# Kernel tuning notes

Hardware: AMD Instinct MI355X
Metric: run time of the kernel (lower is better)

The kernel has to match this reference:

```python
import jax, jax.numpy as jnp
import numpy as np

SEQ, D_IN, D_OUT = 8192, 768, 64


def setup_inputs() -> dict:
    key = jax.random.key(0)
    kx, kq, kk, kv = jax.random.split(key, 4)
    scale = 1.0 / np.sqrt(D_IN)
    return {
        "x": jax.random.normal(kx, (SEQ, D_IN), dtype=jnp.float32),
        # torch Linear weight layout: [d_out, d_in]
        "W_Q": jax.random.uniform(kq, (D_OUT, D_IN), dtype=jnp.float32, minval=-scale, maxval=scale),
        "W_K": jax.random.uniform(kk, (D_OUT, D_IN), dtype=jnp.float32, minval=-scale, maxval=scale),
        "W_V": jax.random.uniform(kv, (D_OUT, D_IN), dtype=jnp.float32, minval=-scale, maxval=scale),
    }


def reference(x, W_Q, W_K, W_V):
    # q,k,v: [seq, d_out]
    q = x @ W_Q.T
    k = x @ W_K.T
    v = x @ W_V.T
    scores = (q @ k.T) / jnp.sqrt(jnp.asarray(k.shape[-1], x.dtype))  # [seq, seq]
    attn = jax.nn.softmax(scores, axis=-1)
    return attn @ v  # [seq, d_out]
```

## Files before the change

### kernel.cpp

```cpp
#include <hip/hip_runtime.h>
#include <hip/hip_bf16.h>
#include <math.h>

#define SEQ 8192
#define DIN 768
#define DOUT 64
#define QSCALE 0.1803368801111214f

typedef __attribute__((ext_vector_type(8))) short short8;
typedef __attribute__((ext_vector_type(4))) short short4v;
typedef __attribute__((ext_vector_type(4))) float floatx4;
typedef __attribute__((ext_vector_type(2))) unsigned int uint2v;

__device__ __forceinline__ void gload16(const void* g, void* l) {
    __builtin_amdgcn_global_load_lds(
        (const __attribute__((address_space(1))) unsigned int*)g,
        (__attribute__((address_space(3))) unsigned int*)l, 16, 0, 0);
}

__device__ __forceinline__ unsigned pack2(float a, float b) {
    __hip_bfloat162 h = __float22bfloat162_rn(make_float2(a, b));
    return *(unsigned*)&h;
}

__device__ __forceinline__ unsigned short bfbits(float f) {
    __hip_bfloat16 h = __float2bfloat16(f);
    return *(unsigned short*)&h;
}

__device__ __forceinline__ float exp2r(float x) {
#if __has_builtin(__builtin_amdgcn_exp2f)
    return __builtin_amdgcn_exp2f(x);
#else
    float r; asm("v_exp_f32 %0, %1" : "=v"(r) : "v"(x)); return r;
#endif
}

__device__ __forceinline__ floatx4 max4(floatx4 a, floatx4 b) {
    floatx4 r;
    r[0] = fmaxf(a[0], b[0]); r[1] = fmaxf(a[1], b[1]);
    r[2] = fmaxf(a[2], b[2]); r[3] = fmaxf(a[3], b[3]);
    return r;
}

__device__ __forceinline__ floatx4 mfma16(short4v a, short4v b, floatx4 c) {
#if __has_builtin(__builtin_amdgcn_mfma_f32_16x16x16bf16_1k)
    return __builtin_amdgcn_mfma_f32_16x16x16bf16_1k(a, b, c, 0, 0, 0);
#else
    asm("v_mfma_f32_16x16x16_bf16 %0, %1, %2, %0" : "+v"(c) : "v"(a), "v"(b));
    return c;
#endif
}

__global__ __launch_bounds__(256) void prep_w(
    const float* __restrict__ Wq, const float* __restrict__ Wk,
    const float* __restrict__ Wv, unsigned short* __restrict__ wbf)
{
    const int i = blockIdx.x * 256 + threadIdx.x;
    const int base = i * 8;
    const int row = base / DIN;
    const int k = base % DIN;
    const float* src = (row < 64)  ? &Wq[(size_t)row * DIN + k]
                     : (row < 128) ? &Wk[(size_t)(row - 64) * DIN + k]
                                   : &Wv[(size_t)(row - 128) * DIN + k];
    const float4 f0 = *(const float4*)src;
    const float4 f1 = *(const float4*)(src + 4);
    uint4 v;
    v.x = pack2(f0.x, f0.y);
    v.y = pack2(f0.z, f0.w);
    v.z = pack2(f1.x, f1.y);
    v.w = pack2(f1.z, f1.w);
    *(uint4*)&wbf[base] = v;
}

__global__ __launch_bounds__(512) void qkv_mfma(
    const float* __restrict__ x, const unsigned short* __restrict__ wbf,
    unsigned short* __restrict__ qbf, unsigned short* __restrict__ kbf,
    unsigned short* __restrict__ vtbf)
{
    __shared__ __align__(16) unsigned char xs[2][64 * 128];
    __shared__ __align__(16) unsigned char wsm[2][192 * 128];

    const int t = threadIdx.x;
    const int l = t & 63;
    const int wid = t >> 6;
    const int h = wid & 3;
    const int ntb = (wid >> 2) * 6;
    const int g = l >> 4;
    const int q4 = l & 15;
    const int row0 = blockIdx.x * 64;

    const int Rx_st = t >> 3;
    const int slx   = t & 7;
    const int Rr    = l >> 3;
    const int sld   = (l & 7) ^ Rr;

    floatx4 acc[6];
#pragma unroll
    for (int i = 0; i < 6; ++i) acc[i] = (floatx4){0.f, 0.f, 0.f, 0.f};

#define STAGE_X(buf, k0)                                                      \
    {                                                                         \
        const float4 a = *(const float4*)&x[(size_t)(row0 + Rx_st) * DIN + (k0) + slx * 8]; \
        const float4 b = *(const float4*)&x[(size_t)(row0 + Rx_st) * DIN + (k0) + slx * 8 + 4]; \
        uint4 v;                                                              \
        v.x = pack2(a.x, a.y); v.y = pack2(a.z, a.w);                         \
        v.z = pack2(b.x, b.y); v.w = pack2(b.z, b.w);                         \
        *(uint4*)&xs[buf][Rx_st * 128 + ((slx ^ (Rx_st & 7)) << 4)] = v;      \
    }

#define STAGE_W(buf, k0)                                                      \
    {                                                                         \
        _Pragma("unroll")                                                     \
        for (int ss = 0; ss < 3; ++ss) {                                      \
            const int s = wid * 3 + ss;                            \
            const int Rw = 8 * s + Rr;                            \
            gload16(&wbf[(size_t)Rw * DIN + (k0) + sld * 8], &wsm[buf][s * 1024]); \
        }                                                                     \
    }

    STAGE_X(0, 0)
    STAGE_W(0, 0)

    int cur = 0;
    for (int kc = 0; kc < 12; ++kc) {
        __syncthreads();

        float4 xa, xb;
        const bool more = (kc + 1 < 12);
        if (more) {
            const int k1 = (kc + 1) * 64;
            STAGE_W(cur ^ 1, k1)
            xa = *(const float4*)&x[(size_t)(row0 + Rx_st) * DIN + k1 + slx * 8];
            xb = *(const float4*)&x[(size_t)(row0 + Rx_st) * DIN + k1 + slx * 8 + 4];
        }

        __builtin_amdgcn_s_setprio(1);
#pragma unroll
        for (int ks = 0; ks < 2; ++ks) {
            const int sl = g + 4 * ks;
            const int Rx = h * 16 + q4;
            const short8 a = *(const short8*)&xs[cur][Rx * 128 + ((sl ^ (Rx & 7)) << 4)];
#pragma unroll
            for (int j = 0; j < 6; ++j) {
                const int Rw = (ntb + j) * 16 + q4;
                const short8 b = *(const short8*)&wsm[cur][Rw * 128 + ((sl ^ (Rw & 7)) << 4)];
                acc[j] = __builtin_amdgcn_mfma_f32_16x16x32_bf16(a, b, acc[j], 0, 0, 0);
            }
        }
        __builtin_amdgcn_s_setprio(0);

        if (more) {
            uint4 v;
            v.x = pack2(xa.x, xa.y); v.y = pack2(xa.z, xa.w);
            v.z = pack2(xb.x, xb.y); v.w = pack2(xb.z, xb.w);
            *(uint4*)&xs[cur ^ 1][Rx_st * 128 + ((slx ^ (Rx_st & 7)) << 4)] = v;
        }
        cur ^= 1;
    }

    const int rb = row0 + h * 16 + (g << 2);
#pragma unroll
    for (int j = 0; j < 6; ++j) {
        const int nt = ntb + j;
#pragma unroll
        for (int r = 0; r < 4; ++r) {
            const float v = acc[j][r];
            const int R = rb + r;
            if (nt < 4) {
                qbf[(size_t)R * 64 + nt * 16 + q4] = bfbits(v * QSCALE);
            } else if (nt < 8) {
                kbf[(size_t)R * 64 + (nt - 4) * 16 + q4] = bfbits(v);
            } else {
                vtbf[(size_t)((nt - 8) * 16 + q4) * SEQ + R] = bfbits(v);
            }
        }
    }
#undef STAGE_X
#undef STAGE_W
}

__global__ __launch_bounds__(256, 4) void flash_mfma(
    const unsigned short* __restrict__ qbf,
    const unsigned short* __restrict__ kbf,
    const unsigned short* __restrict__ vtbf,
    float* __restrict__ opart,
    float* __restrict__ ml,
    int nsplit, int direct)
{
    __shared__ __align__(16) unsigned char lds[32768];
    unsigned char* lkb = lds;
    unsigned char* lvb = lds + 16384;

    const int t = threadIdx.x;
    const int l = t & 63;
    const int g = l >> 4;
    const int q4 = l & 15;
    const int wid = t >> 6;
    const int row0 = blockIdx.x * 64;
    const int split = blockIdx.y;
    const int chunk = SEQ / nsplit;
    const int kbeg = split * chunk;
    const int NT = chunk / 64;

    short8 qf[2];
#pragma unroll
    for (int ks = 0; ks < 2; ++ks)
        qf[ks] = *(const short8*)&qbf[(size_t)(row0 + wid * 16 + q4) * 64 + (g + 4 * ks) * 8];

    {
        const int Rr = l >> 3;
        const int sl = (l & 7) ^ Rr;
#pragma unroll
        for (int ss = 0; ss < 2; ++ss) {
            const int s = wid * 2 + ss;
            const int R = 8 * s + Rr;
            gload16(&kbf[(size_t)(kbeg + R) * 64 + sl * 8], lkb + s * 1024);
            gload16(&vtbf[(size_t)R * SEQ + kbeg + sl * 8], lvb + s * 1024);
        }
    }
    __syncthreads();

    floatx4 oacc[4];
#pragma unroll
    for (int i = 0; i < 4; ++i) oacc[i] = (floatx4){0.f, 0.f, 0.f, 0.f};
    floatx4 l_acc = (floatx4){0.f, 0.f, 0.f, 0.f};
    float m_run = -INFINITY;

    int cur = 0;
    for (int tt = 0; tt < NT; ++tt) {
        const unsigned char* lk = lkb + cur * 8192;
        const unsigned char* lv = lvb + cur * 8192;

        if (tt + 1 < NT) {
            const int kt1 = kbeg + (tt + 1) * 64;
            const int Rr = l >> 3;
            const int sl = (l & 7) ^ Rr;
#pragma unroll
            for (int ss = 0; ss < 2; ++ss) {
                const int s = wid * 2 + ss;
                const int R = 8 * s + Rr;
                gload16(&kbf[(size_t)(kt1 + R) * 64 + sl * 8],
                        lkb + (cur ^ 1) * 8192 + s * 1024);
                gload16(&vtbf[(size_t)R * SEQ + kt1 + sl * 8],
                        lvb + (cur ^ 1) * 8192 + s * 1024);
            }
        }

        floatx4 sacc[4];
#pragma unroll
        for (int i = 0; i < 4; ++i) sacc[i] = (floatx4){0.f, 0.f, 0.f, 0.f};
        __builtin_amdgcn_s_setprio(1);
#pragma unroll
        for (int ks = 0; ks < 2; ++ks) {
            const int sl = g + 4 * ks;
#pragma unroll
            for (int nt = 0; nt < 4; ++nt) {
                const int R = nt * 16 + q4;
                const short8 kf = *(const short8*)&lk[R * 128 + ((sl ^ (R & 7)) << 4)];
                sacc[nt] = __builtin_amdgcn_mfma_f32_16x16x32_bf16(kf, qf[ks], sacc[nt], 0, 0, 0);
            }
        }
        __builtin_amdgcn_s_setprio(0);

        const floatx4 mm = max4(max4(sacc[0], sacc[1]), max4(sacc[2], sacc[3]));
        const float own = fmaxf(fmaxf(mm[0], mm[1]), fmaxf(mm[2], mm[3]));

        if (__any(own > m_run + 8.0f)) {
            float pm = own;
            pm = fmaxf(pm, __shfl_xor(pm, 16));
            pm = fmaxf(pm, __shfl_xor(pm, 32));
            const float mn = fmaxf(m_run, pm);
            const float alpha = exp2r(m_run - mn);
            m_run = mn;
            l_acc *= alpha;
#pragma unroll
            for (int dt = 0; dt < 4; ++dt) oacc[dt] *= alpha;
        }

        floatx4 pv4[4];
#pragma unroll
        for (int nt = 0; nt < 4; ++nt) {
            floatx4 d = sacc[nt];
            d[0] -= m_run; d[1] -= m_run; d[2] -= m_run; d[3] -= m_run;
            pv4[nt][0] = exp2r(d[0]); pv4[nt][1] = exp2r(d[1]);
            pv4[nt][2] = exp2r(d[2]); pv4[nt][3] = exp2r(d[3]);
        }
        l_acc += (pv4[0] + pv4[1]) + (pv4[2] + pv4[3]);

        __builtin_amdgcn_s_setprio(1);
#pragma unroll
        for (int kb = 0; kb < 4; ++kb) {
            const unsigned p0 = pack2(pv4[kb][0], pv4[kb][1]);
            const unsigned p1 = pack2(pv4[kb][2], pv4[kb][3]);
            const short4v bfr = __builtin_bit_cast(short4v, (uint2v){p0, p1});
            const int sl = kb * 2 + (g >> 1);
#pragma unroll
            for (int dt = 0; dt < 4; ++dt) {
                const int R = dt * 16 + q4;
                const short4v a = *(const short4v*)&lv[R * 128 +
                    ((sl ^ (R & 7)) << 4) + ((g & 1) << 3)];
                oacc[dt] = mfma16(a, bfr, oacc[dt]);
            }
        }
        __builtin_amdgcn_s_setprio(0);

        __syncthreads();
        cur ^= 1;
    }

    float l_run = (l_acc[0] + l_acc[1]) + (l_acc[2] + l_acc[3]);
    l_run += __shfl_xor(l_run, 16);
    l_run += __shfl_xor(l_run, 32);

    float* trans = (float*)lds;
    {
        const int qrow = wid * 16 + q4;
        const float sc = direct ? (1.0f / l_run) : 1.0f;
#pragma unroll
        for (int dt = 0; dt < 4; ++dt) {
            floatx4 v = oacc[dt] * sc;
            *(floatx4*)&trans[qrow * 68 + dt * 16 + g * 4] = v;
        }
        if (!direct && l < 16) {
            const size_t mrow = (size_t)split * SEQ + row0 + wid * 16 + l;
            ml[mrow * 2 + 0] = m_run;
            ml[mrow * 2 + 1] = l_run;
        }
    }
    __syncthreads();

    float* outbase = direct ? opart : opart + (size_t)split * SEQ * 64;
#pragma unroll
    for (int it = 0; it < 4; ++it) {
        const int row = it * 16 + (t >> 4);
        const floatx4 v = *(const floatx4*)&trans[row * 68 + (t & 15) * 4];
        *(floatx4*)&outbase[(size_t)(row0 + row) * 64 + (t & 15) * 4] = v;
    }
}

__global__ __launch_bounds__(256) void combine_kernel(
    const float* __restrict__ opart, const float* __restrict__ ml,
    float* __restrict__ out, int nsplit)
{
    const int i4 = blockIdx.x * 256 + threadIdx.x;
    if (i4 >= SEQ * DOUT / 4) return;
    const int row = (i4 * 4) >> 6;

    float M = -INFINITY;
    for (int s = 0; s < nsplit; ++s)
        M = fmaxf(M, ml[((size_t)s * SEQ + row) * 2]);

    float denom = 0.f;
    floatx4 acc = (floatx4){0.f, 0.f, 0.f, 0.f};
    for (int s = 0; s < nsplit; ++s) {
        const float w = exp2r(ml[((size_t)s * SEQ + row) * 2] - M);
        denom += ml[((size_t)s * SEQ + row) * 2 + 1] * w;
        const floatx4 v = *(const floatx4*)&opart[(size_t)s * SEQ * DOUT + i4 * 4];
        acc += v * w;
    }
    acc *= (1.0f / denom);
    *(floatx4*)&out[i4 * 4] = acc;
}

extern "C" void kernel_launch(void* const* d_in, const int* in_sizes, int n_in,
                              void* d_out, int out_size, void* d_ws, size_t ws_size,
                              hipStream_t stream)
{
    const float* x  = (const float*)d_in[0];
    const float* Wq = (const float*)d_in[1];
    const float* Wk = (const float*)d_in[2];
    const float* Wv = (const float*)d_in[3];
    float* out = (float*)d_out;
    unsigned char* ws = (unsigned char*)d_ws;

    const size_t wbf_b = (size_t)192 * DIN * 2;
    const size_t qkv_b = (size_t)SEQ * 64 * 2;
    size_t off = 0;
    unsigned short* wbf  = (unsigned short*)(ws + off); off += wbf_b;
    unsigned short* qbf  = (unsigned short*)(ws + off); off += qkv_b;
    unsigned short* kbf  = (unsigned short*)(ws + off); off += qkv_b;
    unsigned short* vtbf = (unsigned short*)(ws + off); off += qkv_b;

    const size_t per_split = (size_t)SEQ * 64 * 4 + (size_t)SEQ * 2 * 4;
    int nsplit = 0;
    if      (ws_size >= off + 8 * per_split) nsplit = 8;
    else if (ws_size >= off + 4 * per_split) nsplit = 4;
    else if (ws_size >= off + 2 * per_split) nsplit = 2;

    prep_w<<<72, 256, 0, stream>>>(Wq, Wk, Wv, wbf);
    qkv_mfma<<<SEQ / 64, 512, 0, stream>>>(x, wbf, qbf, kbf, vtbf);

    if (nsplit == 0) {
        flash_mfma<<<dim3(SEQ / 64, 1), 256, 0, stream>>>(
            qbf, kbf, vtbf, out, nullptr, 1, 1);
    } else {
        float* opart = (float*)(ws + off);
        float* mlp   = (float*)(ws + off + (size_t)nsplit * SEQ * 64 * 4);
        flash_mfma<<<dim3(SEQ / 64, nsplit), 256, 0, stream>>>(
            qbf, kbf, vtbf, opart, mlp, nsplit, 0);
        combine_kernel<<<(SEQ * DOUT / 4 + 255) / 256, 256, 0, stream>>>(
            opart, mlp, out, nsplit);
    }
}
```

Before: 64.15 us.

## Deepen prefetch pipelines with explicit vmcnt waits and halve QKV tile rows

The QKV projection kernel now uses 32-row tiles with 256 threads, giving twice as many blocks. It prefetches weights and x two stages ahead and replaces __syncthreads with explicit vmcnt/lgkmcnt waits plus raw s_barrier. The flash kernel likewise issues K/V loads two tiles ahead and waits with partial vmcnt counts, so global-to-LDS loads stay in flight across iterations. This aims to hide memory latency and raise parallelism. The cost is correctness that depends on exact outstanding-load counts and barrier placement.

Result: faster. 61.78 us (-3.7%).

```diff
diff --git a/kernel.cpp b/kernel.cpp
--- a/kernel.cpp
+++ b/kernel.cpp
@@ -51,6 +51,12 @@
     return c;
 #endif
 }
+
+#define BAR()       asm volatile("s_barrier" ::: "memory")
+#define WAIT_VM8()  asm volatile("s_waitcnt vmcnt(8)" ::: "memory")
+#define WAIT_VM4()  asm volatile("s_waitcnt vmcnt(4)" ::: "memory")
+#define WAIT_VM0()  asm volatile("s_waitcnt vmcnt(0)" ::: "memory")
+#define WAIT_LGKM() asm volatile("s_waitcnt lgkmcnt(0)" ::: "memory")
 
 __global__ __launch_bounds__(256) void prep_w(
     const float* __restrict__ Wq, const float* __restrict__ Wk,
@@ -73,22 +79,22 @@
     *(uint4*)&wbf[base] = v;
 }
 
-__global__ __launch_bounds__(512) void qkv_mfma(
+__global__ __launch_bounds__(256) void qkv_mfma(
     const float* __restrict__ x, const unsigned short* __restrict__ wbf,
     unsigned short* __restrict__ qbf, unsigned short* __restrict__ kbf,
     unsigned short* __restrict__ vtbf)
 {
-    __shared__ __align__(16) unsigned char xs[2][64 * 128];
+    __shared__ __align__(16) unsigned char xs[2][32 * 128];
     __shared__ __align__(16) unsigned char wsm[2][192 * 128];
 
     const int t = threadIdx.x;
     const int l = t & 63;
     const int wid = t >> 6;
-    const int h = wid & 3;
-    const int ntb = (wid >> 2) * 6;
+    const int h = wid & 1;
+    const int ntb = (wid >> 1) * 6;
     const int g = l >> 4;
     const int q4 = l & 15;
-    const int row0 = blockIdx.x * 64;
+    const int row0 = blockIdx.x * 32;
 
     const int Rx_st = t >> 3;
     const int slx   = t & 7;
@@ -99,41 +105,44 @@
 #pragma unroll
     for (int i = 0; i < 6; ++i) acc[i] = (floatx4){0.f, 0.f, 0.f, 0.f};
 
-#define STAGE_X(buf, k0)                                                      \
-    {                                                                         \
-        const float4 a = *(const float4*)&x[(size_t)(row0 + Rx_st) * DIN + (k0) + slx * 8]; \
-        const float4 b = *(const float4*)&x[(size_t)(row0 + Rx_st) * DIN + (k0) + slx * 8 + 4]; \
-        uint4 v;                                                              \
-        v.x = pack2(a.x, a.y); v.y = pack2(a.z, a.w);                         \
-        v.z = pack2(b.x, b.y); v.w = pack2(b.z, b.w);                         \
-        *(uint4*)&xs[buf][Rx_st * 128 + ((slx ^ (Rx_st & 7)) << 4)] = v;      \
-    }
-
-#define STAGE_W(buf, k0)                                                      \
+#define ISSUE_W(buf, k0)                                                      \
     {                                                                         \
         _Pragma("unroll")                                                     \
-        for (int ss = 0; ss < 3; ++ss) {                                      \
-            const int s = wid * 3 + ss;                            \
+        for (int ss = 0; ss < 6; ++ss) {                                      \
+            const int s = wid * 6 + ss;                            \
             const int Rw = 8 * s + Rr;                            \
             gload16(&wbf[(size_t)Rw * DIN + (k0) + sld * 8], &wsm[buf][s * 1024]); \
         }                                                                     \
     }
-
-    STAGE_X(0, 0)
-    STAGE_W(0, 0)
-
-    int cur = 0;
+#define LOAD_X(dst_a, dst_b, k0)                                              \
+    {                                                                         \
+        dst_a = *(const float4*)&x[(size_t)(row0 + Rx_st) * DIN + (k0) + slx * 8];     \
+        dst_b = *(const float4*)&x[(size_t)(row0 + Rx_st) * DIN + (k0) + slx * 8 + 4]; \
+    }
+#define WRITE_X(buf, src_a, src_b)                                            \
+    {                                                                         \
+        uint4 v;                                                              \
+        v.x = pack2(src_a.x, src_a.y); v.y = pack2(src_a.z, src_a.w);         \
+        v.z = pack2(src_b.x, src_b.y); v.w = pack2(src_b.z, src_b.w);         \
+        *(uint4*)&xs[buf][Rx_st * 128 + ((slx ^ (Rx_st & 7)) << 4)] = v;      \
+    }
+
+    float4 xna, xnb;
+    {
+        float4 a0, b0;
+        ISSUE_W(0, 0)
+        LOAD_X(a0, b0, 0)
+        ISSUE_W(1, 64)
+        LOAD_X(xna, xnb, 64)
+        WRITE_X(0, a0, b0)
+    }
+
+#pragma unroll
     for (int kc = 0; kc < 12; ++kc) {
-        __syncthreads();
-
-        float4 xa, xb;
-        const bool more = (kc + 1 < 12);
-        if (more) {
-            const int k1 = (kc + 1) * 64;
-            STAGE_W(cur ^ 1, k1)
-            xa = *(const float4*)&x[(size_t)(row0 + Rx_st) * DIN + k1 + slx * 8];
-            xb = *(const float4*)&x[(size_t)(row0 + Rx_st) * DIN + k1 + slx * 8 + 4];
-        }
+        const int cur = kc & 1;
+        if (kc < 11) { WAIT_VM8(); } else { WAIT_VM0(); }
+        WAIT_LGKM();
+        BAR();
 
         __builtin_amdgcn_s_setprio(1);
 #pragma unroll
@@ -149,14 +158,16 @@
             }
         }
         __builtin_amdgcn_s_setprio(0);
-
-        if (more) {
-            uint4 v;
-            v.x = pack2(xa.x, xa.y); v.y = pack2(xa.z, xa.w);
-            v.z = pack2(xb.x, xb.y); v.w = pack2(xb.z, xb.w);
-            *(uint4*)&xs[cur ^ 1][Rx_st * 128 + ((slx ^ (Rx_st & 7)) << 4)] = v;
-        }
-        cur ^= 1;
+        BAR();
+
+        if (kc + 1 < 12) {
+            float4 wa = xna, wb = xnb;
+            if (kc + 2 < 12) {
+                ISSUE_W(cur, (kc + 2) * 64)
+                LOAD_X(xna, xnb, (kc + 2) * 64)
+            }
+            WRITE_X(cur ^ 1, wa, wb)
+        }
     }
 
     const int rb = row0 + h * 16 + (g << 2);
@@ -176,8 +187,9 @@
             }
         }
     }
-#undef STAGE_X
-#undef STAGE_W
+#undef ISSUE_W
+#undef LOAD_X
+#undef WRITE_X
 }
 
 __global__ __launch_bounds__(256, 4) void flash_mfma(
@@ -203,23 +215,28 @@
     const int kbeg = split * chunk;
     const int NT = chunk / 64;
 
+#define ISSUE_KV(buf, kt)                                                     \
+    {                                                                         \
+        const int Rr = l >> 3;                                                \
+        const int sl = (l & 7) ^ Rr;                                          \
+        _Pragma("unroll")                                                     \
+        for (int ss = 0; ss < 2; ++ss) {                                      \
+            const int s = wid * 2 + ss;                                       \
+            const int R = 8 * s + Rr;                                         \
+            gload16(&kbf[(size_t)((kt) + R) * 64 + sl * 8],                   \
+                    lkb + (buf) * 8192 + s * 1024);                           \
+            gload16(&vtbf[(size_t)R * SEQ + (kt) + sl * 8],                   \
+                    lvb + (buf) * 8192 + s * 1024);                           \
+        }                                                                     \
+    }
+
     short8 qf[2];
 #pragma unroll
     for (int ks = 0; ks < 2; ++ks)
         qf[ks] = *(const short8*)&qbf[(size_t)(row0 + wid * 16 + q4) * 64 + (g + 4 * ks) * 8];
 
-    {
-        const int Rr = l >> 3;
-        const int sl = (l & 7) ^ Rr;
-#pragma unroll
-        for (int ss = 0; ss < 2; ++ss) {
-            const int s = wid * 2 + ss;
-            const int R = 8 * s + Rr;
-            gload16(&kbf[(size_t)(kbeg + R) * 64 + sl * 8], lkb + s * 1024);
-            gload16(&vtbf[(size_t)R * SEQ + kbeg + sl * 8], lvb + s * 1024);
-        }
-    }
-    __syncthreads();
+    ISSUE_KV(0, kbeg)
+    if (NT > 1) ISSUE_KV(1, kbeg + 64)
 
     floatx4 oacc[4];
 #pragma unroll
@@ -229,23 +246,11 @@
 
     int cur = 0;
     for (int tt = 0; tt < NT; ++tt) {
+        if (tt + 1 < NT) { WAIT_VM4(); } else { WAIT_VM0(); }
+        BAR();
+
         const unsigned char* lk = lkb + cur * 8192;
         const unsigned char* lv = lvb + cur * 8192;
-
-        if (tt + 1 < NT) {
-            const int kt1 = kbeg + (tt + 1) * 64;
-            const int Rr = l >> 3;
-            const int sl = (l & 7) ^ Rr;
-#pragma unroll
-            for (int ss = 0; ss < 2; ++ss) {
-                const int s = wid * 2 + ss;
-                const int R = 8 * s + Rr;
-                gload16(&kbf[(size_t)(kt1 + R) * 64 + sl * 8],
-                        lkb + (cur ^ 1) * 8192 + s * 1024);
-                gload16(&vtbf[(size_t)R * SEQ + kt1 + sl * 8],
-                        lvb + (cur ^ 1) * 8192 + s * 1024);
-            }
-        }
 
         floatx4 sacc[4];
 #pragma unroll
@@ -305,7 +310,8 @@
         }
         __builtin_amdgcn_s_setprio(0);
 
-        __syncthreads();
+        BAR();
+        if (tt + 2 < NT) ISSUE_KV(cur, kbeg + (tt + 2) * 64)
         cur ^= 1;
     }
 
@@ -337,6 +343,7 @@
         const floatx4 v = *(const floatx4*)&trans[row * 68 + (t & 15) * 4];
         *(floatx4*)&outbase[(size_t)(row0 + row) * 64 + (t & 15) * 4] = v;
     }
+#undef ISSUE_KV
 }
 
 __global__ __launch_bounds__(256) void combine_kernel(
@@ -389,7 +396,7 @@
     else if (ws_size >= off + 2 * per_split) nsplit = 2;
 
     prep_w<<<72, 256, 0, stream>>>(Wq, Wk, Wv, wbf);
-    qkv_mfma<<<SEQ / 64, 512, 0, stream>>>(x, wbf, qbf, kbf, vtbf);
+    qkv_mfma<<<SEQ / 32, 256, 0, stream>>>(x, wbf, qbf, kbf, vtbf);
 
     if (nsplit == 0) {
         flash_mfma<<<dim3(SEQ / 64, 1), 256, 0, stream>>>(
```
